# Kernel optimization log

Measured on AMD Instinct MI355X. Metric: run time of the kernel, lower is better.

Reference implementation:

```python
import jax, jax.numpy as jnp
import numpy as np

B, C, HW, P = 8, 128, 50176, 128  # batch, channels, flattened spatial, num parcels

def setup_inputs() -> dict:
    key = jax.random.key(0)
    k1, k2 = jax.random.split(key)
    x = jax.random.normal(k1, (B, C, HW), dtype=jnp.float32)
    # 0/1 parcel assignment mask [b, num_parcs, hw]
    parcel_mask_batch = jax.random.randint(k2, (B, P, HW), 0, 2).astype(jnp.float32)
    return {"x": x, "parcel_mask_batch": parcel_mask_batch}

def reference(x, parcel_mask_batch):
    # torch: for each i, x[i] @ mask[i].T  -> stacked [b, c, num_parcs]
    # out[b, c, p] = sum_hw x[b, c, hw] * mask[b, p, hw]
    return jnp.einsum('bch,bph->bcp', x, parcel_mask_batch)
```

## Files before the change

### kernel.cpp

```cpp
#include <hip/hip_runtime.h>
#include <hip/hip_bf16.h>

typedef float f32x4 __attribute__((ext_vector_type(4)));
typedef short short8 __attribute__((ext_vector_type(8)));

#define BATCH 8
#define CH    128
#define HWN   50176
#define PN    128
#define KSPLIT 32
#define KWIN  1568
#define BK    32
#define NST   49

__device__ __forceinline__ ushort f2bf_rn(float f){
  uint u = __float_as_uint(f);
  u += 0x7FFFu + ((u >> 16) & 1u);
  return (ushort)(u >> 16);
}
__device__ __forceinline__ float bf2f(ushort h){
  return __uint_as_float(((uint)h) << 16);
}

__device__ __forceinline__ short8 cvt8_trunc(f32x4 a, f32x4 b){
  union{ short8 v; ushort u[8]; } r;
  r.u[0]=(ushort)(__float_as_uint(a.x)>>16); r.u[1]=(ushort)(__float_as_uint(a.y)>>16);
  r.u[2]=(ushort)(__float_as_uint(a.z)>>16); r.u[3]=(ushort)(__float_as_uint(a.w)>>16);
  r.u[4]=(ushort)(__float_as_uint(b.x)>>16); r.u[5]=(ushort)(__float_as_uint(b.y)>>16);
  r.u[6]=(ushort)(__float_as_uint(b.z)>>16); r.u[7]=(ushort)(__float_as_uint(b.w)>>16);
  return r.v;
}

__device__ __forceinline__ void cvt8_hilo(f32x4 a, f32x4 b, short8& h8, short8& l8){
  union{ short8 v; ushort u[8]; } h, l;
  float f[8] = {a.x,a.y,a.z,a.w,b.x,b.y,b.z,b.w};
  #pragma unroll
  for(int j=0;j<8;++j){
    ushort hh = (ushort)(__float_as_uint(f[j]) >> 16);
    h.u[j] = hh;
    l.u[j] = f2bf_rn(f[j] - bf2f(hh));
  }
  h8 = h.v; l8 = l.v;
}

__device__ __forceinline__ void gload16(const float* g, float* l){
  __builtin_amdgcn_global_load_lds(
      (const __attribute__((address_space(1))) void*)g,
      (__attribute__((address_space(3))) void*)l, 16, 0, 0);
}

__device__ __forceinline__ f32x4 lds_read4(const float* base, int r, int slot){
  return *(const f32x4*)(base + r*32 + ((slot ^ (r&7)) << 2));
}

template<int EPI>
__global__ __launch_bounds__(512, 1)
void raggr_kernel(const float* __restrict__ X, const float* __restrict__ Mk,
                  float* __restrict__ OUT, float* __restrict__ PART){
  __shared__ float lds[4 * 8192];

  const int tid  = threadIdx.x;
  const int b    = blockIdx.x >> 5;
  const int s    = blockIdx.x & 31;
  const int lane = tid & 63;
  const int w    = tid >> 6;
  const int wrow = (w >> 2) * 64;
  const int wcol = (w & 3) * 32;

  const size_t base = (size_t)b * CH * HWN + (size_t)s * KWIN;
  const f32x4 z4 = {0.f,0.f,0.f,0.f};

  f32x4 acc[4][2];
  #pragma unroll
  for(int m=0;m<4;++m){ acc[m][0]=z4; acc[m][1]=z4; }

  const int lrow = lane >> 3;
  const int kq   = (lane & 7) ^ lrow;
  const float* SRC = (w >= 4) ? Mk : X;
  const float* ps[4];
  float* ld0[4];
  #pragma unroll
  for(int i=0;i<4;++i){
    int r = (w & 3)*32 + i*8 + lrow;
    ps[i]  = SRC + base + (size_t)r * HWN + kq*4;
    ld0[i] = lds + ((w >= 4) ? 4096 : 0) + ((w & 3)*32 + i*8)*32;
  }

  #define STAGE(tt) {                                                         \
    float* dst = ld0[0] + ((tt) & 3) * 8192;                                  \
    const size_t go = (size_t)(tt) * BK;                                      \
    gload16(ps[0] + go, dst);                                                 \
    gload16(ps[1] + go, ld0[1] + ((tt) & 3) * 8192);                          \
    gload16(ps[2] + go, ld0[2] + ((tt) & 3) * 8192);                          \
    gload16(ps[3] + go, ld0[3] + ((tt) & 3) * 8192);                          \
  }

  #define COMPUTE(tt) {                                                       \
    const float* Xb = lds + ((tt) & 3) * 8192;                                \
    const float* Mb = Xb + 4096;                                              \
    const int l15 = lane & 15;                                                \
    const int s0  = (lane >> 4) * 2;                                          \
    short8 bf[2], ah[4], al[4];                                               \
    _Pragma("unroll")                                                         \
    for(int n=0;n<2;++n){                                                     \
      int r = wcol + n*16 + l15;                                              \
      bf[n] = cvt8_trunc(lds_read4(Mb, r, s0), lds_read4(Mb, r, s0+1));       \
    }                                                                         \
    _Pragma("unroll")                                                         \
    for(int m=0;m<4;++m){                                                     \
      int r = wrow + m*16 + l15;                                              \
      cvt8_hilo(lds_read4(Xb, r, s0), lds_read4(Xb, r, s0+1), ah[m], al[m]);  \
    }                                                                         \
    _Pragma("unroll")                                                         \
    for(int m=0;m<4;++m)                                                      \
      _Pragma("unroll")                                                       \
      for(int n=0;n<2;++n){                                                   \
        acc[m][n] = __builtin_amdgcn_mfma_f32_16x16x32_bf16(ah[m], bf[n], acc[m][n], 0,0,0); \
        acc[m][n] = __builtin_amdgcn_mfma_f32_16x16x32_bf16(al[m], bf[n], acc[m][n], 0,0,0); \
      }                                                                       \
  }

  STAGE(0); STAGE(1); STAGE(2);

  #pragma unroll 1
  for(int t=0; t<NST; ++t){
    if(t < NST-2)       asm volatile("s_waitcnt vmcnt(8)" ::: "memory");
    else if(t == NST-2) asm volatile("s_waitcnt vmcnt(4)" ::: "memory");
    else                asm volatile("s_waitcnt vmcnt(0)" ::: "memory");
    __builtin_amdgcn_s_barrier();
    if(t+3 < NST) STAGE(t+3);
    COMPUTE(t);
  }

  if(EPI == 0){
    #pragma unroll
    for(int m=0;m<4;++m){
      int row0 = wrow + m*16 + ((lane >> 4) << 2);
      #pragma unroll
      for(int n=0;n<2;++n){
        int col = wcol + n*16 + (lane & 15);
        #pragma unroll
        for(int j=0;j<4;++j)
          PART[(size_t)b*524288 + (size_t)(row0+j)*4096 + s*128 + col] = acc[m][n][j];
      }
    }
  } else {
    float* o = OUT + (size_t)b * 16384;
    #pragma unroll
    for(int m=0;m<4;++m){
      int row0 = wrow + m*16 + ((lane >> 4) << 2);
      #pragma unroll
      for(int n=0;n<2;++n){
        int col = wcol + n*16 + (lane & 15);
        #pragma unroll
        for(int j=0;j<4;++j) atomicAdd(&o[(size_t)(row0+j)*128 + col], acc[m][n][j]);
      }
    }
  }
  #undef STAGE
  #undef COMPUTE
}

__global__ void reduce_kernel(const float* __restrict__ PART, float* __restrict__ OUT){
  int bid = blockIdx.x;
  int b   = bid >> 6;
  int c   = (bid & 63)*2 + (threadIdx.x >> 7);
  int p   = threadIdx.x & 127;
  size_t base_ = (size_t)b*524288 + (size_t)c*4096 + p;
  float sum = 0.f;
  #pragma unroll 8
  for(int k=0;k<32;++k) sum += PART[base_ + k*128];
  OUT[(size_t)b*16384 + c*128 + p] = sum;
}

__global__ void zero_kernel(float* __restrict__ OUT){
  int idx = blockIdx.x * 256 + threadIdx.x;
  if(idx < BATCH*CH*PN) OUT[idx] = 0.f;
}

extern "C" void kernel_launch(void* const* d_in, const int* in_sizes, int n_in,
                              void* d_out, int out_size, void* d_ws, size_t ws_size,
                              hipStream_t stream){
  const float* X  = (const float*)d_in[0];
  const float* Mk = (const float*)d_in[1];
  float* O = (float*)d_out;

  const size_t part_bytes = (size_t)BATCH * KSPLIT * CH * PN * sizeof(float);
  if(ws_size >= part_bytes && d_ws != nullptr){
    float* part = (float*)d_ws;
    raggr_kernel<0><<<dim3(BATCH*KSPLIT), dim3(512), 0, stream>>>(X, Mk, O, part);
    reduce_kernel<<<dim3(512), dim3(256), 0, stream>>>(part, O);
  } else {
    zero_kernel<<<dim3(512), dim3(256), 0, stream>>>(O);
    raggr_kernel<1><<<dim3(BATCH*KSPLIT), dim3(512), 0, stream>>>(X, Mk, O, nullptr);
  }
}
```

Before: 421.7 us.

## Load X directly into registers and stage mask as pre-converted bf16 in LDS

Restructures the main kernel so each wave owns 16 channel rows of X and computes all 128 parcels. X is loaded straight from global memory into registers with a 4-deep register prefetch. The mask is loaded into registers, converted to bf16 once, and written to a double-buffered swizzled LDS tile, with one barrier per 224-wide K chunk instead of one per 32-wide step. This removes repeated per-wave conversion of the mask and cuts LDS traffic and barrier count. In exchange it raises register pressure with large mreg and xr arrays, uses 128 KB of LDS, and drops the async global-to-LDS loads.

```diff
diff --git a/kernel.cpp b/kernel.cpp
--- a/kernel.cpp
+++ b/kernel.cpp
@@ -10,8 +10,9 @@
 #define PN    128
 #define KSPLIT 32
 #define KWIN  1568
-#define BK    32
-#define NST   49
+#define BK    224
+#define NST   7
+#define NKS   49
 
 __device__ __forceinline__ ushort f2bf_rn(float f){
   uint u = __float_as_uint(f);
@@ -43,122 +44,113 @@
   h8 = h.v; l8 = l.v;
 }
 
-__device__ __forceinline__ void gload16(const float* g, float* l){
-  __builtin_amdgcn_global_load_lds(
-      (const __attribute__((address_space(1))) void*)g,
-      (__attribute__((address_space(3))) void*)l, 16, 0, 0);
-}
-
-__device__ __forceinline__ f32x4 lds_read4(const float* base, int r, int slot){
-  return *(const f32x4*)(base + r*32 + ((slot ^ (r&7)) << 2));
-}
-
 template<int EPI>
 __global__ __launch_bounds__(512, 1)
 void raggr_kernel(const float* __restrict__ X, const float* __restrict__ Mk,
                   float* __restrict__ OUT, float* __restrict__ PART){
-  __shared__ float lds[4 * 8192];
+  __shared__ char smem[2 * 65536];
 
   const int tid  = threadIdx.x;
   const int b    = blockIdx.x >> 5;
   const int s    = blockIdx.x & 31;
   const int lane = tid & 63;
   const int w    = tid >> 6;
-  const int wrow = (w >> 2) * 64;
-  const int wcol = (w & 3) * 32;
+  const int l15  = lane & 15;
+  const int hi4  = lane >> 4;
 
   const size_t base = (size_t)b * CH * HWN + (size_t)s * KWIN;
   const f32x4 z4 = {0.f,0.f,0.f,0.f};
 
-  f32x4 acc[4][2];
+  const float* pX = X + base + (size_t)(w*16 + l15) * HWN + hi4*8;
+
+  const int mr = tid >> 2;
+  const int mc = tid & 3;
+  const int r7 = mr & 7;
+  const float* pM = Mk + base + (size_t)mr * HWN + mc*56;
+  char* mwr = smem + mr*512;
+
+  f32x4 acc[8];
   #pragma unroll
-  for(int m=0;m<4;++m){ acc[m][0]=z4; acc[m][1]=z4; }
+  for(int n=0;n<8;++n) acc[n] = z4;
 
-  const int lrow = lane >> 3;
-  const int kq   = (lane & 7) ^ lrow;
-  const float* SRC = (w >= 4) ? Mk : X;
-  const float* ps[4];
-  float* ld0[4];
+  f32x4 xr[4][2];
+  f32x4 mreg[14];
+
+  #define ISSUE_X(g) {                                                        \
+    xr[(g)&3][0] = *(const f32x4*)(pX + (size_t)(g)*32);                      \
+    xr[(g)&3][1] = *(const f32x4*)(pX + (size_t)(g)*32 + 4);                  \
+  }
+  #define ISSUE_M(t) {                                                        \
+    _Pragma("unroll")                                                         \
+    for(int i=0;i<14;++i)                                                     \
+      mreg[i] = *(const f32x4*)(pM + (size_t)(t)*BK + i*4);                   \
+  }
+  #define CVTW_M(buf) {                                                      \
+    char* dst = mwr + (buf)*65536;                                            \
+    _Pragma("unroll")                                                         \
+    for(int i=0;i<7;++i){                                                     \
+      short8 v = cvt8_trunc(mreg[2*i], mreg[2*i+1]);                          \
+      *(short8*)(dst + (((mc*7 + i) ^ r7) << 4)) = v;                         \
+    } }
+
+  ISSUE_M(0);
+  ISSUE_X(0); ISSUE_X(1); ISSUE_X(2); ISSUE_X(3);
+  CVTW_M(0);
+  ISSUE_M(1);
+  __syncthreads();
+
   #pragma unroll
-  for(int i=0;i<4;++i){
-    int r = (w & 3)*32 + i*8 + lrow;
-    ps[i]  = SRC + base + (size_t)r * HWN + kq*4;
-    ld0[i] = lds + ((w >= 4) ? 4096 : 0) + ((w & 3)*32 + i*8)*32;
-  }
+  for(int g=0; g<NKS; ++g){
+    const int t  = g / 7;
+    const int ks = g % 7;
+    const char* Mb = smem + (t & 1) * 65536;
 
-  #define STAGE(tt) {                                                         \
-    float* dst = ld0[0] + ((tt) & 3) * 8192;                                  \
-    const size_t go = (size_t)(tt) * BK;                                      \
-    gload16(ps[0] + go, dst);                                                 \
-    gload16(ps[1] + go, ld0[1] + ((tt) & 3) * 8192);                          \
-    gload16(ps[2] + go, ld0[2] + ((tt) & 3) * 8192);                          \
-    gload16(ps[3] + go, ld0[3] + ((tt) & 3) * 8192);                          \
-  }
+    short8 bf[8];
+    #pragma unroll
+    for(int n=0;n<8;++n){
+      int p = n*16 + l15;
+      bf[n] = *(const short8*)(Mb + p*512 + (((ks*4 + hi4) ^ (p & 7)) << 4));
+    }
+    short8 ah, al;
+    cvt8_hilo(xr[g&3][0], xr[g&3][1], ah, al);
 
-  #define COMPUTE(tt) {                                                       \
-    const float* Xb = lds + ((tt) & 3) * 8192;                                \
-    const float* Mb = Xb + 4096;                                              \
-    const int l15 = lane & 15;                                                \
-    const int s0  = (lane >> 4) * 2;                                          \
-    short8 bf[2], ah[4], al[4];                                               \
-    _Pragma("unroll")                                                         \
-    for(int n=0;n<2;++n){                                                     \
-      int r = wcol + n*16 + l15;                                              \
-      bf[n] = cvt8_trunc(lds_read4(Mb, r, s0), lds_read4(Mb, r, s0+1));       \
-    }                                                                         \
-    _Pragma("unroll")                                                         \
-    for(int m=0;m<4;++m){                                                     \
-      int r = wrow + m*16 + l15;                                              \
-      cvt8_hilo(lds_read4(Xb, r, s0), lds_read4(Xb, r, s0+1), ah[m], al[m]);  \
-    }                                                                         \
-    _Pragma("unroll")                                                         \
-    for(int m=0;m<4;++m)                                                      \
-      _Pragma("unroll")                                                       \
-      for(int n=0;n<2;++n){                                                   \
-        acc[m][n] = __builtin_amdgcn_mfma_f32_16x16x32_bf16(ah[m], bf[n], acc[m][n], 0,0,0); \
-        acc[m][n] = __builtin_amdgcn_mfma_f32_16x16x32_bf16(al[m], bf[n], acc[m][n], 0,0,0); \
-      }                                                                       \
-  }
+    #pragma unroll
+    for(int n=0;n<8;++n){
+      acc[n] = __builtin_amdgcn_mfma_f32_16x16x32_bf16(ah, bf[n], acc[n], 0,0,0);
+      acc[n] = __builtin_amdgcn_mfma_f32_16x16x32_bf16(al, bf[n], acc[n], 0,0,0);
+    }
 
-  STAGE(0); STAGE(1); STAGE(2);
+    if(g + 4 < NKS) ISSUE_X(g + 4);
 
-  #pragma unroll 1
-  for(int t=0; t<NST; ++t){
-    if(t < NST-2)       asm volatile("s_waitcnt vmcnt(8)" ::: "memory");
-    else if(t == NST-2) asm volatile("s_waitcnt vmcnt(4)" ::: "memory");
-    else                asm volatile("s_waitcnt vmcnt(0)" ::: "memory");
-    __builtin_amdgcn_s_barrier();
-    if(t+3 < NST) STAGE(t+3);
-    COMPUTE(t);
+    if(ks == 6 && t < NST-1){
+      CVTW_M((t+1) & 1);
+      if(t < NST-2) ISSUE_M(t+2);
+      __syncthreads();
+    }
   }
 
   if(EPI == 0){
     #pragma unroll
-    for(int m=0;m<4;++m){
-      int row0 = wrow + m*16 + ((lane >> 4) << 2);
+    for(int n=0;n<8;++n){
+      int col  = n*16 + l15;
+      int row0 = w*16 + hi4*4;
       #pragma unroll
-      for(int n=0;n<2;++n){
-        int col = wcol + n*16 + (lane & 15);
-        #pragma unroll
-        for(int j=0;j<4;++j)
-          PART[(size_t)b*524288 + (size_t)(row0+j)*4096 + s*128 + col] = acc[m][n][j];
-      }
+      for(int j=0;j<4;++j)
+        PART[(size_t)b*524288 + (size_t)(row0+j)*4096 + s*128 + col] = acc[n][j];
     }
   } else {
     float* o = OUT + (size_t)b * 16384;
     #pragma unroll
-    for(int m=0;m<4;++m){
-      int row0 = wrow + m*16 + ((lane >> 4) << 2);
+    for(int n=0;n<8;++n){
+      int col  = n*16 + l15;
+      int row0 = w*16 + hi4*4;
       #pragma unroll
-      for(int n=0;n<2;++n){
-        int col = wcol + n*16 + (lane & 15);
-        #pragma unroll
-        for(int j=0;j<4;++j) atomicAdd(&o[(size_t)(row0+j)*128 + col], acc[m][n][j]);
-      }
+      for(int j=0;j<4;++j) atomicAdd(&o[(size_t)(row0+j)*128 + col], acc[n][j]);
     }
   }
-  #undef STAGE
-  #undef COMPUTE
+  #undef ISSUE_X
+  #undef ISSUE_M
+  #undef CVTW_M
 }
 
 __global__ void reduce_kernel(const float* __restrict__ PART, float* __restrict__ OUT){
```

Result: faster. 411.9 us (-2.3%).
